# Optimization experiments

Hardware: AMD Instinct MI355X
Metric: run time of the kernel (lower is better)

## Reference

```python
import jax, jax.numpy as jnp
import numpy as np

B, C, H, W = 8, 512, 96, 96
C8 = C // 8


def conv1x1(x, w, b):
    # x: (B,Cin,H,W), w: (Cout,Cin), b: (Cout,)
    return jnp.einsum('bchw,oc->bohw', x, w) + b[None, :, None, None]


def setup_inputs() -> dict:
    key = jax.random.key(0)
    ks = jax.random.split(key, 12)
    s = 0.05
    return {
        'x_exmplar': jax.random.normal(ks[0], (B, C, H, W), jnp.float32),
        'x_query': jax.random.normal(ks[1], (B, C, H, W), jnp.float32),
        'Wq': jax.random.normal(ks[2], (C8, C), jnp.float32) * s,
        'bq': jax.random.normal(ks[3], (C8,), jnp.float32) * s,
        'Wk': jax.random.normal(ks[4], (C8, C), jnp.float32) * s,
        'bk': jax.random.normal(ks[5], (C8,), jnp.float32) * s,
        'Wv': jax.random.normal(ks[6], (C, C), jnp.float32) * s,
        'bv': jax.random.normal(ks[7], (C,), jnp.float32) * s,
        'Wqv': jax.random.normal(ks[8], (C, C), jnp.float32) * s,
        'bqv': jax.random.normal(ks[9], (C,), jnp.float32) * s,
        'gamma1': jax.random.normal(ks[10], (1,), jnp.float32) * 0.5,
        'gamma2': jax.random.normal(ks[11], (1,), jnp.float32) * 0.5,
    }


def reference(x_exmplar, x_query, Wq, bq, Wk, bk, Wv, bv, Wqv, bqv, gamma1, gamma2):
    Bq, Cq, Hh, Ww = x_query.shape
    q = conv1x1(x_query, Wq, bq)        # (B,C8,H,W)
    k = conv1x1(x_exmplar, Wk, bk)      # (B,C8,H,W)
    v = conv1x1(x_exmplar, Wv, bv)      # (B,C,H,W)
    qv = conv1x1(x_query, Wqv, bqv)     # (B,C,H,W)

    # Criss-cross energies. energy_H masks the self position (INF diag).
    eH = jnp.einsum('bchw,bcjw->bhwj', q, k)            # (B,H,W,H)
    eye = jnp.eye(Hh, dtype=bool)                        # (H,H)
    eH = jnp.where(eye[:, None, :], -jnp.inf, eH)        # mask h==j
    eW = jnp.einsum('bchw,bchj->bhwj', q, k)             # (B,H,W,W)

    att = jax.nn.softmax(jnp.concatenate([eH, eW], axis=3), axis=3)
    att_H, att_W = att[..., :Hh], att[..., Hh:]          # (B,H,W,H),(B,H,W,W)

    out_H = jnp.einsum('bcjw,bhwj->bchw', v, att_H)
    out_W = jnp.einsum('bchj,bhwj->bchw', v, att_W)
    qout_H = jnp.einsum('bcjw,bhwj->bchw', qv, att_H)
    qout_W = jnp.einsum('bchj,bhwj->bchw', qv, att_W)

    # Diagonal (LR/RL) terms. Note: torch.diagonal of the transposed map equals
    # the diagonal itself, so energy_RL == energy_LR (faithful to original).
    qd = jnp.diagonal(q, axis1=2, axis2=3)               # (B,C8,D)
    kd = jnp.diagonal(k, axis1=2, axis2=3)
    vd = jnp.diagonal(v, axis1=2, axis2=3)               # (B,C,D)
    qvd = jnp.diagonal(qv, axis1=2, axis2=3)
    e_LR = jnp.einsum('bci,bcj->bij', kd, qd)            # (B,D,D)

    # softmax over a size-1 trailing axis (as in the original): yields ones,
    # broadcast-added over the width dim.
    out_LR = jax.nn.softmax(jnp.einsum('bcd,bdj->bcj', vd, e_LR)[..., None], axis=3)
    out_RL = jax.nn.softmax(jnp.einsum('bcd,bdj->bcj', vd, e_LR)[..., None], axis=3)
    qout_LR = jax.nn.softmax(jnp.einsum('bcd,bdj->bcj', qvd, e_LR)[..., None], axis=3)
    qout_RL = jax.nn.softmax(jnp.einsum('bcd,bdj->bcj', qvd, e_LR)[..., None], axis=3)

    examplar_att = out_H + out_W + out_LR + out_RL       # (B,C,H,W) via broadcast
    query_att = qout_H + qout_W + qout_LR + qout_RL
    return (gamma1 * examplar_att + x_exmplar, gamma2 * query_att + x_query)
```

## Files before the change

kernel.cpp:

```cpp
#include <hip/hip_runtime.h>
#include <math.h>

#define C_   512
#define C8_  64
#define HH   96
#define WW   96
#define PP   9216
#define CP   4718592
#define C8P  589824
#define ATTN 1769472

typedef __attribute__((ext_vector_type(4))) float f32x4;
typedef __attribute__((ext_vector_type(8))) __bf16 bf16x8;
typedef __attribute__((ext_vector_type(8))) unsigned short ushort8;
typedef __attribute__((ext_vector_type(4))) unsigned short ushort4v;
typedef __attribute__((ext_vector_type(2))) unsigned short ushort2v;
typedef __attribute__((ext_vector_type(2))) float float2v;

__device__ __forceinline__ float bf2f(unsigned short u) {
    union { unsigned u; float f; } x; x.u = ((unsigned)u) << 16; return x.f;
}
__device__ __forceinline__ unsigned short f2bf(float f) {
    union { float f; unsigned u; } x; x.f = f;
    unsigned r = x.u + 0x7fffu + ((x.u >> 16) & 1u);
    return (unsigned short)(r >> 16);
}
__device__ __forceinline__ void gload16(const void* g, void* l) {
    __builtin_amdgcn_global_load_lds(
        (const __attribute__((address_space(1))) unsigned int*)g,
        (__attribute__((address_space(3))) unsigned int*)l, 16, 0, 0);
}

__global__ __launch_bounds__(256) void cast_w(
    const float* __restrict__ Wv, const float* __restrict__ Wqv,
    const float* __restrict__ Wq, const float* __restrict__ Wk,
    unsigned short* __restrict__ oV, unsigned short* __restrict__ oQV,
    unsigned short* __restrict__ oQ, unsigned short* __restrict__ oK)
{
    int y = blockIdx.y;
    int n = (y < 2) ? 262144 : 32768;
    const float* s = (y == 0) ? Wv : (y == 1) ? Wqv : (y == 2) ? Wq : Wk;
    unsigned short* d = (y == 0) ? oV : (y == 1) ? oQV : (y == 2) ? oQ : oK;
    int i = (blockIdx.x * 256 + threadIdx.x) * 4;
    if (i < n) {
        float4 v = *(const float4*)(s + i);
        ushort4v o = { f2bf(v.x), f2bf(v.y), f2bf(v.z), f2bf(v.w) };
        *(ushort4v*)(d + i) = o;
    }
}

__global__ __launch_bounds__(256) void cast_transpose_cp(
    const float* __restrict__ xq, const float* __restrict__ xe,
    unsigned short* __restrict__ xTq, unsigned short* __restrict__ xTe)
{
    int zz = blockIdx.z;
    int which = zz & 1;
    size_t b = zz >> 1;
    const float* xb = (which ? xe : xq) + b * (size_t)CP;
    unsigned short* xTb = (which ? xTe : xTq) + b * (size_t)CP;
    int p0 = blockIdx.x * 64, c0 = blockIdx.y * 64;

    __shared__ unsigned short T[64][65];
    int t = threadIdx.x;
    int pp = t & 31, cg = t >> 5;
#pragma unroll
    for (int i = 0; i < 8; ++i) {
        int c = cg + 8 * i;
        float2v v = *(const float2v*)(xb + (size_t)(c0 + c) * PP + p0 + pp * 2);
        T[c][pp * 2] = f2bf(v.x);
        T[c][pp * 2 + 1] = f2bf(v.y);
    }
    __syncthreads();
    int cp = t & 31;
#pragma unroll
    for (int i = 0; i < 8; ++i) {
        int e = t + 256 * i;
        int p = e >> 5;
        ushort2v o = { T[cp * 2][p], T[cp * 2 + 1][p] };
        *(ushort2v*)(xTb + (size_t)(p0 + p) * C_ + c0 + cp * 2) = o;
    }
}

__global__ __launch_bounds__(256) void gemm_qk(
    const unsigned short* __restrict__ Wqb, const unsigned short* __restrict__ Wkb,
    const unsigned short* __restrict__ xTq, const unsigned short* __restrict__ xTe,
    const float* __restrict__ bq, const float* __restrict__ bk,
    unsigned short* __restrict__ qout, unsigned short* __restrict__ kout)
{
    int sel = blockIdx.y;
    const unsigned short* A = sel ? Wkb : Wqb;
    const float* bias = sel ? bk : bq;
    int p0 = blockIdx.x * 128;
    size_t b = blockIdx.z;
    const unsigned short* Bb = (sel ? xTe : xTq) + b * (size_t)CP;
    unsigned short* outb = (sel ? kout : qout) + b * (size_t)C8P;

    __shared__ __align__(16) unsigned short Asm[64 * 32];
    __shared__ __align__(16) unsigned short Bsm[128 * 32];

    int tid = threadIdx.x;
    int lane = tid & 63, wid = tid >> 6;
    int wr = wid >> 1, wc = wid & 1;
    int l15 = lane & 15, l4 = lane >> 4;
    f32x4 acc[2][4] = {};

    for (int k0 = 0; k0 < 512; k0 += 32) {
        int c = tid;
        gload16(A + (size_t)(c >> 2) * 512 + k0 + (c & 3) * 8, Asm + c * 8);
        gload16(Bb + (size_t)(p0 + (c >> 2)) * 512 + k0 + (c & 3) * 8, Bsm + c * 8);
        int cb = tid + 256;
        gload16(Bb + (size_t)(p0 + (cb >> 2)) * 512 + k0 + (cb & 3) * 8, Bsm + cb * 8);
        __syncthreads();
        bf16x8 af[2], bfr[4];
#pragma unroll
        for (int m = 0; m < 2; ++m)
            af[m] = *(const bf16x8*)&Asm[(wr * 32 + m * 16 + l15) * 32 + l4 * 8];
#pragma unroll
        for (int n = 0; n < 4; ++n)
            bfr[n] = *(const bf16x8*)&Bsm[(wc * 64 + n * 16 + l15) * 32 + l4 * 8];
#pragma unroll
        for (int m = 0; m < 2; ++m)
#pragma unroll
            for (int n = 0; n < 4; ++n)
                acc[m][n] = __builtin_amdgcn_mfma_f32_16x16x32_bf16(af[m], bfr[n], acc[m][n], 0, 0, 0);
        __syncthreads();
    }
#pragma unroll
    for (int m = 0; m < 2; ++m)
#pragma unroll
        for (int n = 0; n < 4; ++n) {
            int pcol = p0 + wc * 64 + n * 16 + l15;
#pragma unroll
            for (int r = 0; r < 4; ++r) {
                int orow = wr * 32 + m * 16 + l4 * 4 + r;
                outb[(size_t)orow * PP + pcol] = f2bf(acc[m][n][r] + bias[orow]);
            }
        }
}

__global__ __launch_bounds__(256) void thw_b(
    const unsigned short* __restrict__ in, unsigned short* __restrict__ out)
{
    size_t m = blockIdx.x;
    const unsigned short* im = in + m * (size_t)PP;
    unsigned short* om = out + m * (size_t)PP;
    __shared__ unsigned short T[96][97];
    int t = threadIdx.x;
#pragma unroll
    for (int i = 0; i < 18; ++i) {
        int v = t + 256 * i;
        int r = v / 48, pp = v - r * 48;
        ushort2v u = *(const ushort2v*)(im + r * 96 + pp * 2);
        T[r][pp * 2] = u.x;
        T[r][pp * 2 + 1] = u.y;
    }
    __syncthreads();
#pragma unroll
    for (int i = 0; i < 18; ++i) {
        int v = t + 256 * i;
        int w = v / 48, hh = v - w * 48;
        ushort2v o = { T[hh * 2][w], T[hh * 2 + 1][w] };
        *(ushort2v*)(om + w * 96 + hh * 2) = o;
    }
}

__global__ __launch_bounds__(256) void scores_kernel(
    const unsigned short* __restrict__ qT, const unsigned short* __restrict__ kT,
    const unsigned short* __restrict__ q, const unsigned short* __restrict__ k,
    unsigned short* __restrict__ attb, float* __restrict__ rsum0, float* __restrict__ rsum1)
{
    int s = blockIdx.x;
    int ori = blockIdx.y;
    size_t b = blockIdx.z;
    const unsigned short* qs = (ori ? q : qT) + b * (size_t)C8P;
    const unsigned short* ks = (ori ? k : kT) + b * (size_t)C8P;
    unsigned short* ab = attb + b * (size_t)ATTN;
    float* rs = (ori ? rsum1 : rsum0) + b * (size_t)PP;

    __shared__ float Qs[64][97];
    __shared__ float Ks[64][97];
    int t = threadIdx.x;
    for (int v = t; v < 64 * 12; v += 256) {
        int c = v / 12, gg = v - c * 12;
        size_t gi = (size_t)c * PP + (size_t)s * 96 + gg * 8;
        ushort8 uq = *(const ushort8*)(qs + gi);
        ushort8 uk = *(const ushort8*)(ks + gi);
#pragma unroll
        for (int kk = 0; kk < 8; ++kk) {
            Qs[c][gg * 8 + kk] = bf2f(uq[kk]);
            Ks[c][gg * 8 + kk] = bf2f(uk[kk]);
        }
    }
    __syncthreads();
    int tx = t & 15, ty = t >> 4;
    float acc[6][6] = {};
    for (int c = 0; c < 64; ++c) {
        float qf[6], kf[6];
#pragma unroll
        for (int i = 0; i < 6; ++i) { qf[i] = Qs[c][ty + 16 * i]; kf[i] = Ks[c][tx + 16 * i]; }
#pragma unroll
        for (int i = 0; i < 6; ++i)
#pragma unroll
            for (int j = 0; j < 6; ++j) acc[i][j] = fmaf(qf[i], kf[j], acc[i][j]);
    }
#pragma unroll
    for (int i = 0; i < 6; ++i) {
        int m = ty + 16 * i;
        size_t row = ori ? ((size_t)s * 96 + m) : ((size_t)m * 96 + s);
        unsigned short* rowp = ab + row * 192 + (ori ? 96 : 0);
        float part = 0.0f;
#pragma unroll
        for (int j = 0; j < 6; ++j) {
            int jj = tx + 16 * j;
            float e = (!ori && jj == m) ? 0.0f : __expf(acc[i][j] - 20.0f);
            part += e;
            rowp[jj] = f2bf(e);
        }
#pragma unroll
        for (int off = 1; off < 16; off <<= 1) part += __shfl_xor(part, off);
        if (tx == 0) rs[row] = part;
    }
}

template<int ORI>
__global__ __launch_bounds__(512) void apply_mfma(
    const unsigned short* __restrict__ xT_e, const unsigned short* __restrict__ xT_q,
    unsigned short* __restrict__ yT_e, unsigned short* __restrict__ yT_q,
    const unsigned short* __restrict__ attb,
    const float* __restrict__ rsum0, const float* __restrict__ rsum1)
{
    int s = blockIdx.x;
    int path = blockIdx.y >> 1, ct = blockIdx.y & 1;
    int c0 = ct * 256;
    size_t b = blockIdx.z;
    const unsigned short* X = (path ? xT_q : xT_e) + b * (size_t)CP;
    unsigned short* Y = (path ? yT_q : yT_e) + b * (size_t)CP;
    const unsigned short* ab = attb + b * (size_t)ATTN;
    const float* r0 = rsum0 + b * (size_t)PP;
    const float* r1 = rsum1 + b * (size_t)PP;

    __shared__ __align__(16) unsigned short Att[96][104];
    __shared__ __align__(16) unsigned short Xs[256][104];

    int tid = threadIdx.x;
    for (int v = tid; v < 96 * 12; v += 512) {
        int r = v / 12, gg = v - r * 12;
        size_t base = ORI ? ((size_t)(s * 96 + r) * 192 + 96) : ((size_t)(r * 96 + s) * 192);
        *(ushort8*)&Att[r][gg * 8] = *(const ushort8*)(ab + base + gg * 8);
    }
    for (int v = tid; v < 96 * 32; v += 512) {
        int j = v >> 5, cc = v & 31;
        size_t pj = ORI ? ((size_t)s * 96 + j) : ((size_t)j * 96 + s);
        ushort8 u = *(const ushort8*)(X + pj * C_ + c0 + cc * 8);
        int js = j ^ ((cc & 3) << 3);
#pragma unroll
        for (int e = 0; e < 8; ++e) Xs[cc * 8 + e][js] = u[e];
    }
    __syncthreads();

    int lane = tid & 63, wid = tid >> 6;
    int wm = wid >> 2, wn = wid & 3;
    int l15 = lane & 15, l4 = lane >> 4;
    f32x4 acc[3][4] = {};
#pragma unroll
    for (int k = 0; k < 3; ++k) {
        bf16x8 a[3], xx[4];
#pragma unroll
        for (int mi = 0; mi < 3; ++mi)
            a[mi] = *(const bf16x8*)&Att[wm * 48 + mi * 16 + l15][k * 32 + l4 * 8];
#pragma unroll
        for (int ni = 0; ni < 4; ++ni) {
            int row = wn * 64 + ni * 16 + l15;
            int gsw = (k * 4 + l4) ^ ((row >> 3) & 3);
            xx[ni] = *(const bf16x8*)&Xs[row][gsw * 8];
        }
#pragma unroll
        for (int mi = 0; mi < 3; ++mi)
#pragma unroll
            for (int ni = 0; ni < 4; ++ni)
                acc[mi][ni] = __builtin_amdgcn_mfma_f32_16x16x32_bf16(a[mi], xx[ni], acc[mi][ni], 0, 0, 0);
    }

#pragma unroll
    for (int mi = 0; mi < 3; ++mi) {
#pragma unroll
        for (int r = 0; r < 4; ++r) {
            int mrow = wm * 48 + mi * 16 + l4 * 4 + r;
            size_t p = ORI ? ((size_t)s * 96 + mrow) : ((size_t)mrow * 96 + s);
            float rinv = 0.0f;
            if (ORI) rinv = 1.0f / (r0[p] + r1[p]);
            size_t base = p * C_ + c0;
#pragma unroll
            for (int ni = 0; ni < 4; ++ni) {
                size_t idx = base + wn * 64 + ni * 16 + l15;
                if (ORI == 0) {
                    Y[idx] = f2bf(acc[mi][ni][r]);
                } else {
                    float tot = bf2f(Y[idx]) + acc[mi][ni][r];
                    Y[idx] = f2bf(tot * rinv);
                }
            }
        }
    }
}

__global__ __launch_bounds__(256) void gemm_out(
    const unsigned short* __restrict__ Wvb, const unsigned short* __restrict__ Wqvb,
    const unsigned short* __restrict__ yT_e, const unsigned short* __restrict__ yT_q,
    const float* __restrict__ bv, const float* __restrict__ bqv,
    const float* __restrict__ xe, const float* __restrict__ xq,
    const float* __restrict__ g1, const float* __restrict__ g2,
    float* __restrict__ o0, float* __restrict__ o1)
{
    int yy = blockIdx.y;
    int path = yy >> 2, ot = yy & 3;
    const unsigned short* A = path ? Wqvb : Wvb;
    const float* bias = path ? bqv : bv;
    int p0 = blockIdx.x * 128;
    int o0r = ot * 128;
    size_t b = blockIdx.z;
    const unsigned short* Bb = (path ? yT_q : yT_e) + b * (size_t)CP;
    const float* xb = (path ? xq : xe) + b * (size_t)CP;
    float* ob = (path ? o1 : o0) + b * (size_t)CP;
    float gam = (path ? g2 : g1)[0];

    __shared__ __align__(16) unsigned short Asm[2][128 * 64];
    __shared__ __align__(16) unsigned short Bsm[2][128 * 64];

    int tid = threadIdx.x;
    int lane = tid & 63, wid = tid >> 6;
    int wr = wid >> 1, wc = wid & 1;
    int l15 = lane & 15, l4 = lane >> 4;
    f32x4 acc[4][4] = {};

#pragma unroll
    for (int i = 0; i < 4; ++i) {
        int ch = tid + i * 256;
        int row = ch >> 3, slot = ch & 7;
        int gs = slot ^ (row & 7);
        gload16(A + (size_t)(o0r + row) * 512 + gs * 8, Asm[0] + ch * 8);
        gload16(Bb + (size_t)(p0 + row) * 512 + gs * 8, Bsm[0] + ch * 8);
    }
    __syncthreads();

#pragma unroll
    for (int k = 0; k < 8; ++k) {
        int cur = k & 1;
        if (k < 7) {
            int k0n = (k + 1) * 64;
            int nxt = cur ^ 1;
#pragma unroll
            for (int i = 0; i < 4; ++i) {
                int ch = tid + i * 256;
                int row = ch >> 3, slot = ch & 7;
                int gs = slot ^ (row & 7);
                gload16(A + (size_t)(o0r + row) * 512 + k0n + gs * 8, Asm[nxt] + ch * 8);
                gload16(Bb + (size_t)(p0 + row) * 512 + k0n + gs * 8, Bsm[nxt] + ch * 8);
            }
        }
#pragma unroll
        for (int ks = 0; ks < 2; ++ks) {
            bf16x8 af[4], bfr[4];
#pragma unroll
            for (int m = 0; m < 4; ++m) {
                int row = wr * 64 + m * 16 + l15;
                int sl = (ks * 4 + l4) ^ (row & 7);
                af[m] = *(const bf16x8*)&Asm[cur][row * 64 + sl * 8];
            }
#pragma unroll
            for (int n = 0; n < 4; ++n) {
                int row = wc * 64 + n * 16 + l15;
                int sl = (ks * 4 + l4) ^ (row & 7);
                bfr[n] = *(const bf16x8*)&Bsm[cur][row * 64 + sl * 8];
            }
#pragma unroll
            for (int m = 0; m < 4; ++m)
#pragma unroll
                for (int n = 0; n < 4; ++n)
                    acc[m][n] = __builtin_amdgcn_mfma_f32_16x16x32_bf16(af[m], bfr[n], acc[m][n], 0, 0, 0);
        }
        __syncthreads();
    }

#pragma unroll
    for (int m = 0; m < 4; ++m)
#pragma unroll
        for (int n = 0; n < 4; ++n) {
            int pcol = p0 + wc * 64 + n * 16 + l15;
#pragma unroll
            for (int r = 0; r < 4; ++r) {
                int orow = o0r + wr * 64 + m * 16 + l4 * 4 + r;
                size_t idx = (size_t)orow * PP + pcol;
                float val = acc[m][n][r] + bias[orow];
                ob[idx] = gam * (val + 2.0f) + xb[idx];
            }
        }
}

extern "C" void kernel_launch(void* const* d_in, const int* in_sizes, int n_in,
                              void* d_out, int out_size, void* d_ws, size_t ws_size,
                              hipStream_t stream)
{
    const float* x_ex = (const float*)d_in[0];
    const float* x_q  = (const float*)d_in[1];
    const float* Wq   = (const float*)d_in[2];
    const float* bq   = (const float*)d_in[3];
    const float* Wk   = (const float*)d_in[4];
    const float* bk   = (const float*)d_in[5];
    const float* Wv   = (const float*)d_in[6];
    const float* bv   = (const float*)d_in[7];
    const float* Wqv  = (const float*)d_in[8];
    const float* bqv  = (const float*)d_in[9];
    const float* g1   = (const float*)d_in[10];
    const float* g2   = (const float*)d_in[11];
    float* out0 = (float*)d_out;
    float* out1 = out0 + (size_t)8 * CP;

    unsigned short* hp = (unsigned short*)d_ws;
    unsigned short* Wvb  = hp; hp += 262144;
    unsigned short* Wqvb = hp; hp += 262144;
    unsigned short* Wqb  = hp; hp += 32768;
    unsigned short* Wkb  = hp; hp += 32768;
    size_t head = (size_t)(hp - (unsigned short*)d_ws) * 2;

    size_t perB = 4ull * CP + (size_t)ATTN + 4ull * C8P + 4ull * PP;
    int g = 8;
    while (g > 1 && head + (size_t)g * perB * 2 > ws_size) g >>= 1;

    unsigned short* p = hp;
    unsigned short* xT_e = p; p += (size_t)g * CP;
    unsigned short* xT_q = p; p += (size_t)g * CP;
    unsigned short* yT_e = p; p += (size_t)g * CP;
    unsigned short* yT_q = p; p += (size_t)g * CP;
    unsigned short* attb = p; p += (size_t)g * ATTN;
    unsigned short* qb   = p; p += (size_t)g * C8P;
    unsigned short* kb   = p; p += (size_t)g * C8P;
    unsigned short* qTb  = p; p += (size_t)g * C8P;
    unsigned short* kTb  = p; p += (size_t)g * C8P;
    float* rsum0 = (float*)p; p += (size_t)g * PP * 2;
    float* rsum1 = (float*)p; p += (size_t)g * PP * 2;

    cast_w<<<dim3(256, 4), 256, 0, stream>>>(Wv, Wqv, Wq, Wk, Wvb, Wqvb, Wqb, Wkb);

    for (int b0 = 0; b0 < 8; b0 += g) {
        const float* xe = x_ex + (size_t)b0 * CP;
        const float* xq = x_q  + (size_t)b0 * CP;
        float* o0 = out0 + (size_t)b0 * CP;
        float* o1 = out1 + (size_t)b0 * CP;

        cast_transpose_cp<<<dim3(144, 8, 2 * g), 256, 0, stream>>>(xq, xe, xT_q, xT_e);
        gemm_qk<<<dim3(72, 2, g), 256, 0, stream>>>(Wqb, Wkb, xT_q, xT_e, bq, bk, qb, kb);
        thw_b<<<dim3(2 * g * 64), 256, 0, stream>>>(qb, qTb);
        scores_kernel<<<dim3(96, 2, g), 256, 0, stream>>>(qTb, kTb, qb, kb, attb, rsum0, rsum1);
        apply_mfma<0><<<dim3(96, 4, g), 512, 0, stream>>>(xT_e, xT_q, yT_e, yT_q, attb, rsum0, rsum1);
        apply_mfma<1><<<dim3(96, 4, g), 512, 0, stream>>>(xT_e, xT_q, yT_e, yT_q, attb, rsum0, rsum1);
        gemm_out<<<dim3(72, 8, g), 256, 0, stream>>>(Wvb, Wqvb, yT_e, yT_q, bv, bqv,
                                                     xe, xq, g1, g2, o0, o1);
    }
}
```

Measured before the change: 587.6 us.

## Fuse criss-cross score computation into attention-apply kernels, dropping global attention buffer

Merges the scores kernel with the two MFMA apply kernels, so each block computes its own 96x96 exp-energy tile straight into shared memory and then applies it to both channel halves. This removes the global bf16 attention buffer and the rsum1 array, trading their write and reread for recomputing the scores once per path (exemplar and query). The ORI=1 pass keeps its row sums in shared memory, and LDS is reused between the fp32 Q/K staging and the X tile. Fewer launches and lower workspace may allow a larger batch group g, but the scores work is doubled and each block now loops over the two channel tiles serially.

```diff
diff --git a/kernel.cpp b/kernel.cpp
--- a/kernel.cpp
+++ b/kernel.cpp
@@ -8,7 +8,6 @@
 #define PP   9216
 #define CP   4718592
 #define C8P  589824
-#define ATTN 1769472
 
 typedef __attribute__((ext_vector_type(4))) float f32x4;
 typedef __attribute__((ext_vector_type(8))) __bf16 bf16x8;
@@ -164,143 +163,135 @@
     }
 }
 
-__global__ __launch_bounds__(256) void scores_kernel(
-    const unsigned short* __restrict__ qT, const unsigned short* __restrict__ kT,
-    const unsigned short* __restrict__ q, const unsigned short* __restrict__ k,
-    unsigned short* __restrict__ attb, float* __restrict__ rsum0, float* __restrict__ rsum1)
+template<int ORI>
+__global__ __launch_bounds__(512) void fused_sa(
+    const unsigned short* __restrict__ qsrc, const unsigned short* __restrict__ ksrc,
+    const unsigned short* __restrict__ xT_e, const unsigned short* __restrict__ xT_q,
+    unsigned short* __restrict__ yT_e, unsigned short* __restrict__ yT_q,
+    float* __restrict__ rsum0)
 {
     int s = blockIdx.x;
-    int ori = blockIdx.y;
+    int path = blockIdx.y;
     size_t b = blockIdx.z;
-    const unsigned short* qs = (ori ? q : qT) + b * (size_t)C8P;
-    const unsigned short* ks = (ori ? k : kT) + b * (size_t)C8P;
-    unsigned short* ab = attb + b * (size_t)ATTN;
-    float* rs = (ori ? rsum1 : rsum0) + b * (size_t)PP;
-
-    __shared__ float Qs[64][97];
-    __shared__ float Ks[64][97];
+    const unsigned short* qs = qsrc + b * (size_t)C8P;
+    const unsigned short* ks = ksrc + b * (size_t)C8P;
+    const unsigned short* X = (path ? xT_q : xT_e) + b * (size_t)CP;
+    unsigned short* Y = (path ? yT_q : yT_e) + b * (size_t)CP;
+    float* rs0 = rsum0 + b * (size_t)PP;
+
+    __shared__ __align__(16) char U[53248];
+    float* Qs = (float*)U;
+    float* Ks = Qs + 64 * 97;
+    unsigned short* Xs = (unsigned short*)U;
+    __shared__ __align__(16) unsigned short Att[96][104];
+    __shared__ float rsl[96];
+
     int t = threadIdx.x;
-    for (int v = t; v < 64 * 12; v += 256) {
+    int lane = t & 63, wid = t >> 6;
+
+    for (int v = t; v < 64 * 12; v += 512) {
         int c = v / 12, gg = v - c * 12;
         size_t gi = (size_t)c * PP + (size_t)s * 96 + gg * 8;
         ushort8 uq = *(const ushort8*)(qs + gi);
         ushort8 uk = *(const ushort8*)(ks + gi);
 #pragma unroll
-        for (int kk = 0; kk < 8; ++kk) {
-            Qs[c][gg * 8 + kk] = bf2f(uq[kk]);
-            Ks[c][gg * 8 + kk] = bf2f(uk[kk]);
+        for (int e = 0; e < 8; ++e) {
+            Qs[c * 97 + gg * 8 + e] = bf2f(uq[e]);
+            Ks[c * 97 + gg * 8 + e] = bf2f(uk[e]);
         }
     }
     __syncthreads();
+
     int tx = t & 15, ty = t >> 4;
-    float acc[6][6] = {};
+    float acc[3][6] = {};
     for (int c = 0; c < 64; ++c) {
-        float qf[6], kf[6];
-#pragma unroll
-        for (int i = 0; i < 6; ++i) { qf[i] = Qs[c][ty + 16 * i]; kf[i] = Ks[c][tx + 16 * i]; }
-#pragma unroll
-        for (int i = 0; i < 6; ++i)
+        float qf[3], kf[6];
+#pragma unroll
+        for (int i = 0; i < 3; ++i) qf[i] = Qs[c * 97 + ty + 32 * i];
+#pragma unroll
+        for (int j = 0; j < 6; ++j) kf[j] = Ks[c * 97 + tx + 16 * j];
+#pragma unroll
+        for (int i = 0; i < 3; ++i)
 #pragma unroll
             for (int j = 0; j < 6; ++j) acc[i][j] = fmaf(qf[i], kf[j], acc[i][j]);
     }
 #pragma unroll
-    for (int i = 0; i < 6; ++i) {
-        int m = ty + 16 * i;
-        size_t row = ori ? ((size_t)s * 96 + m) : ((size_t)m * 96 + s);
-        unsigned short* rowp = ab + row * 192 + (ori ? 96 : 0);
+    for (int i = 0; i < 3; ++i) {
+        int m = ty + 32 * i;
         float part = 0.0f;
 #pragma unroll
         for (int j = 0; j < 6; ++j) {
             int jj = tx + 16 * j;
-            float e = (!ori && jj == m) ? 0.0f : __expf(acc[i][j] - 20.0f);
+            float e = (ORI == 0 && jj == m) ? 0.0f : __expf(acc[i][j] - 20.0f);
             part += e;
-            rowp[jj] = f2bf(e);
+            Att[m][jj] = f2bf(e);
         }
 #pragma unroll
         for (int off = 1; off < 16; off <<= 1) part += __shfl_xor(part, off);
-        if (tx == 0) rs[row] = part;
-    }
-}
-
-template<int ORI>
-__global__ __launch_bounds__(512) void apply_mfma(
-    const unsigned short* __restrict__ xT_e, const unsigned short* __restrict__ xT_q,
-    unsigned short* __restrict__ yT_e, unsigned short* __restrict__ yT_q,
-    const unsigned short* __restrict__ attb,
-    const float* __restrict__ rsum0, const float* __restrict__ rsum1)
-{
-    int s = blockIdx.x;
-    int path = blockIdx.y >> 1, ct = blockIdx.y & 1;
-    int c0 = ct * 256;
-    size_t b = blockIdx.z;
-    const unsigned short* X = (path ? xT_q : xT_e) + b * (size_t)CP;
-    unsigned short* Y = (path ? yT_q : yT_e) + b * (size_t)CP;
-    const unsigned short* ab = attb + b * (size_t)ATTN;
-    const float* r0 = rsum0 + b * (size_t)PP;
-    const float* r1 = rsum1 + b * (size_t)PP;
-
-    __shared__ __align__(16) unsigned short Att[96][104];
-    __shared__ __align__(16) unsigned short Xs[256][104];
-
-    int tid = threadIdx.x;
-    for (int v = tid; v < 96 * 12; v += 512) {
-        int r = v / 12, gg = v - r * 12;
-        size_t base = ORI ? ((size_t)(s * 96 + r) * 192 + 96) : ((size_t)(r * 96 + s) * 192);
-        *(ushort8*)&Att[r][gg * 8] = *(const ushort8*)(ab + base + gg * 8);
-    }
-    for (int v = tid; v < 96 * 32; v += 512) {
-        int j = v >> 5, cc = v & 31;
-        size_t pj = ORI ? ((size_t)s * 96 + j) : ((size_t)j * 96 + s);
-        ushort8 u = *(const ushort8*)(X + pj * C_ + c0 + cc * 8);
-        int js = j ^ ((cc & 3) << 3);
-#pragma unroll
-        for (int e = 0; e < 8; ++e) Xs[cc * 8 + e][js] = u[e];
+        if (tx == 0) {
+            if (ORI == 0) rs0[(size_t)m * 96 + s] = part;
+            else          rsl[m] = part;
+        }
     }
     __syncthreads();
 
-    int lane = tid & 63, wid = tid >> 6;
     int wm = wid >> 2, wn = wid & 3;
     int l15 = lane & 15, l4 = lane >> 4;
-    f32x4 acc[3][4] = {};
-#pragma unroll
-    for (int k = 0; k < 3; ++k) {
-        bf16x8 a[3], xx[4];
-#pragma unroll
-        for (int mi = 0; mi < 3; ++mi)
-            a[mi] = *(const bf16x8*)&Att[wm * 48 + mi * 16 + l15][k * 32 + l4 * 8];
-#pragma unroll
-        for (int ni = 0; ni < 4; ++ni) {
-            int row = wn * 64 + ni * 16 + l15;
-            int gsw = (k * 4 + l4) ^ ((row >> 3) & 3);
-            xx[ni] = *(const bf16x8*)&Xs[row][gsw * 8];
-        }
-#pragma unroll
-        for (int mi = 0; mi < 3; ++mi)
-#pragma unroll
-            for (int ni = 0; ni < 4; ++ni)
-                acc[mi][ni] = __builtin_amdgcn_mfma_f32_16x16x32_bf16(a[mi], xx[ni], acc[mi][ni], 0, 0, 0);
-    }
-
-#pragma unroll
-    for (int mi = 0; mi < 3; ++mi) {
-#pragma unroll
-        for (int r = 0; r < 4; ++r) {
-            int mrow = wm * 48 + mi * 16 + l4 * 4 + r;
-            size_t p = ORI ? ((size_t)s * 96 + mrow) : ((size_t)mrow * 96 + s);
-            float rinv = 0.0f;
-            if (ORI) rinv = 1.0f / (r0[p] + r1[p]);
-            size_t base = p * C_ + c0;
+#pragma unroll
+    for (int ct = 0; ct < 2; ++ct) {
+        int c0 = ct * 256;
+        for (int v = t; v < 96 * 32; v += 512) {
+            int j = v >> 5, cc = v & 31;
+            size_t pj = ORI ? ((size_t)s * 96 + j) : ((size_t)j * 96 + s);
+            ushort8 u = *(const ushort8*)(X + pj * C_ + c0 + cc * 8);
+            int js = j ^ ((cc & 3) << 3);
+#pragma unroll
+            for (int e = 0; e < 8; ++e) Xs[(cc * 8 + e) * 104 + js] = u[e];
+        }
+        __syncthreads();
+
+        f32x4 pacc[3][4] = {};
+#pragma unroll
+        for (int k = 0; k < 3; ++k) {
+            bf16x8 a[3], xx[4];
+#pragma unroll
+            for (int mi = 0; mi < 3; ++mi)
+                a[mi] = *(const bf16x8*)&Att[wm * 48 + mi * 16 + l15][k * 32 + l4 * 8];
 #pragma unroll
             for (int ni = 0; ni < 4; ++ni) {
-                size_t idx = base + wn * 64 + ni * 16 + l15;
-                if (ORI == 0) {
-                    Y[idx] = f2bf(acc[mi][ni][r]);
-                } else {
-                    float tot = bf2f(Y[idx]) + acc[mi][ni][r];
-                    Y[idx] = f2bf(tot * rinv);
+                int row = wn * 64 + ni * 16 + l15;
+                int gsw = (k * 4 + l4) ^ ((row >> 3) & 3);
+                xx[ni] = *(const bf16x8*)&Xs[row * 104 + gsw * 8];
+            }
+#pragma unroll
+            for (int mi = 0; mi < 3; ++mi)
+#pragma unroll
+                for (int ni = 0; ni < 4; ++ni)
+                    pacc[mi][ni] = __builtin_amdgcn_mfma_f32_16x16x32_bf16(a[mi], xx[ni], pacc[mi][ni], 0, 0, 0);
+        }
+
+#pragma unroll
+        for (int mi = 0; mi < 3; ++mi) {
+#pragma unroll
+            for (int r = 0; r < 4; ++r) {
+                int mrow = wm * 48 + mi * 16 + l4 * 4 + r;
+                size_t p = ORI ? ((size_t)s * 96 + mrow) : ((size_t)mrow * 96 + s);
+                float rinv = 0.0f;
+                if (ORI) rinv = 1.0f / (rs0[p] + rsl[mrow]);
+                size_t base = p * C_ + c0;
+#pragma unroll
+                for (int ni = 0; ni < 4; ++ni) {
+                    size_t idx = base + wn * 64 + ni * 16 + l15;
+                    if (ORI == 0) {
+                        Y[idx] = f2bf(pacc[mi][ni][r]);
+                    } else {
+                        float tot = bf2f(Y[idx]) + pacc[mi][ni][r];
+                        Y[idx] = f2bf(tot * rinv);
+                    }
                 }
             }
         }
+        __syncthreads();
     }
 }
 
@@ -423,7 +414,7 @@
     unsigned short* Wkb  = hp; hp += 32768;
     size_t head = (size_t)(hp - (unsigned short*)d_ws) * 2;
 
-    size_t perB = 4ull * CP + (size_t)ATTN + 4ull * C8P + 4ull * PP;
+    size_t perB = 4ull * CP + 4ull * C8P + 2ull * PP;
     int g = 8;
     while (g > 1 && head + (size_t)g * perB * 2 > ws_size) g >>= 1;
 
@@ -432,13 +423,11 @@
     unsigned short* xT_q = p; p += (size_t)g * CP;
     unsigned short* yT_e = p; p += (size_t)g * CP;
     unsigned short* yT_q = p; p += (size_t)g * CP;
-    unsigned short* attb = p; p += (size_t)g * ATTN;
     unsigned short* qb   = p; p += (size_t)g * C8P;
     unsigned short* kb   = p; p += (size_t)g * C8P;
     unsigned short* qTb  = p; p += (size_t)g * C8P;
     unsigned short* kTb  = p; p += (size_t)g * C8P;
     float* rsum0 = (float*)p; p += (size_t)g * PP * 2;
-    float* rsum1 = (float*)p; p += (size_t)g * PP * 2;
 
     cast_w<<<dim3(256, 4), 256, 0, stream>>>(Wv, Wqv, Wq, Wk, Wvb, Wqvb, Wqb, Wkb);
 
@@ -451,9 +440,8 @@
         cast_transpose_cp<<<dim3(144, 8, 2 * g), 256, 0, stream>>>(xq, xe, xT_q, xT_e);
         gemm_qk<<<dim3(72, 2, g), 256, 0, stream>>>(Wqb, Wkb, xT_q, xT_e, bq, bk, qb, kb);
         thw_b<<<dim3(2 * g * 64), 256, 0, stream>>>(qb, qTb);
-        scores_kernel<<<dim3(96, 2, g), 256, 0, stream>>>(qTb, kTb, qb, kb, attb, rsum0, rsum1);
-        apply_mfma<0><<<dim3(96, 4, g), 512, 0, stream>>>(xT_e, xT_q, yT_e, yT_q, attb, rsum0, rsum1);
-        apply_mfma<1><<<dim3(96, 4, g), 512, 0, stream>>>(xT_e, xT_q, yT_e, yT_q, attb, rsum0, rsum1);
+        fused_sa<0><<<dim3(96, 2, g), 512, 0, stream>>>(qTb, kTb, xT_e, xT_q, yT_e, yT_q, rsum0);
+        fused_sa<1><<<dim3(96, 2, g), 512, 0, stream>>>(qb,  kb,  xT_e, xT_q, yT_e, yT_q, rsum0);
         gemm_out<<<dim3(72, 8, g), 256, 0, stream>>>(Wvb, Wqvb, yT_e, yT_q, bv, bqv,
                                                      xe, xq, g1, g2, o0, o1);
     }
```

After: 645.5 us. 1.1x slower.
